# Kernel tuning notes

Hardware: AMD Instinct MI355X
Metric: run time of the kernel (lower is better)

The kernel has to match this reference:

```python
import jax, jax.numpy as jnp
import numpy as np
from math import log

MODEL_DIM = 512
NUM_HEADS = 8
DIM_HEAD = 64
INNER = NUM_HEADS * DIM_HEAD
B, L = 8, 1024
EPS = 1e-5


def setup_inputs() -> dict:
    key = jax.random.key(0)
    ks = jax.random.split(key, 9)
    x = jax.random.normal(ks[0], (B, L, MODEL_DIM), dtype=jnp.float32)
    gamma = jnp.ones((MODEL_DIM,), jnp.float32)
    beta = jnp.zeros((MODEL_DIM,), jnp.float32)
    w_qkv = jax.random.normal(ks[1], (3 * INNER, MODEL_DIM), jnp.float32) * (MODEL_DIM ** -0.5)
    b_qkv = jnp.zeros((3 * INNER,), jnp.float32)
    w_pos = jax.random.normal(ks[2], (INNER, MODEL_DIM), jnp.float32) * (MODEL_DIM ** -0.5)
    w_out = jax.random.normal(ks[3], (MODEL_DIM, INNER), jnp.float32) * (INNER ** -0.5)
    b_out = jnp.zeros((MODEL_DIM,), jnp.float32)
    # xavier_uniform for (num_heads, dim_head)
    bound = (6.0 / (NUM_HEADS + DIM_HEAD)) ** 0.5
    u_bias = jax.random.uniform(ks[4], (NUM_HEADS, DIM_HEAD), jnp.float32, -bound, bound)
    v_bias = jax.random.uniform(ks[5], (NUM_HEADS, DIM_HEAD), jnp.float32, -bound, bound)
    return {"x": x, "gamma": gamma, "beta": beta, "w_qkv": w_qkv, "b_qkv": b_qkv,
            "w_pos": w_pos, "w_out": w_out, "b_out": b_out, "u_bias": u_bias, "v_bias": v_bias}


def _rel_pos_emb(seq_len, d):
    # (L, D): (i - j) scaled by sinusoid frequencies, then cos on even cols, sin on odd cols
    rel = (jnp.arange(seq_len, dtype=jnp.float32)[:, None]
           - jnp.arange(d, dtype=jnp.float32)[None, :])
    freqs = jnp.exp(-jnp.arange(0, 2 * d, 2, dtype=jnp.float32) * (log(10000.0) / MODEL_DIM))
    angle = rel * freqs[None, :]
    even = (jnp.arange(d) % 2) == 0
    return jnp.where(even[None, :], jnp.cos(angle), jnp.sin(angle))  # (L, D)


def reference(x, gamma, beta, w_qkv, b_qkv, w_pos, w_out, b_out, u_bias, v_bias):
    b, l, d = x.shape
    h, dh = NUM_HEADS, DIM_HEAD
    # LayerNorm
    mu = jnp.mean(x, axis=-1, keepdims=True)
    var = jnp.mean(jnp.square(x - mu), axis=-1, keepdims=True)
    xn = (x - mu) * jax.lax.rsqrt(var + EPS) * gamma + beta
    # relative position embedding, identical per batch element
    pe = _rel_pos_emb(l, d)                      # (L, D)
    pos = (pe @ w_pos.T).reshape(l, h, dh)       # (L, H, Dh)
    pos = jnp.transpose(pos, (1, 0, 2))          # (H, L, Dh)
    # qkv
    qkv = xn @ w_qkv.T + b_qkv                   # (B, L, 3*inner)
    q, k, v = jnp.split(qkv, 3, axis=-1)
    def to_heads(t):
        return jnp.transpose(t.reshape(b, l, h, dh), (0, 2, 1, 3))  # (B,H,L,Dh)
    q, k, v = to_heads(q), to_heads(k), to_heads(v)
    scale = dh ** -0.5
    content = jnp.einsum('bhld,bhmd->bhlm', q + u_bias[None, :, None, :], k)
    pos_score = jnp.einsum('bhld,hmd->bhlm', q + v_bias[None, :, None, :], pos)
    attn = jax.nn.softmax((content + pos_score) * scale, axis=-1)
    out = jnp.einsum('bhlm,bhmd->bhld', attn, v)
    out = jnp.transpose(out, (0, 2, 1, 3)).reshape(b, l, h * dh)
    return out @ w_out.T + b_out  # dropout p=0.0 -> identity
```

## Files before the change

### kernel.cpp

```cpp
#include <hip/hip_runtime.h>
#include <math.h>

static constexpr int Bn = 8, Ln = 1024, Dm = 512, Hn = 8, DhN = 64;

typedef short bf16x8 __attribute__((ext_vector_type(8)));
typedef float f32x4 __attribute__((ext_vector_type(4)));
typedef _Float16 f16x4 __attribute__((ext_vector_type(4)));
typedef _Float16 f16x8 __attribute__((ext_vector_type(8)));
typedef unsigned int u32x4 __attribute__((ext_vector_type(4)));
typedef unsigned short u16x8 __attribute__((ext_vector_type(8)));

#define QSCALE 0.1803368801111137f

static __device__ __forceinline__ unsigned short f2b(float f) {
  union { float f; unsigned int u; } x;
  x.f = f;
  unsigned int u = x.u;
  unsigned int r = (u + 0x7FFFu + ((u >> 16) & 1u)) >> 16;
  return (unsigned short)r;
}
static __device__ __forceinline__ float b2f(unsigned short u) {
  union { unsigned int u; float f; } x;
  x.u = ((unsigned int)u) << 16;
  return x.f;
}

#define GLDS16(g, l)                                                        \
  __builtin_amdgcn_global_load_lds((const __attribute__((address_space(1))) void*)(g), \
                                   (__attribute__((address_space(3))) void*)(l), 16, 0, 0)

__global__ __launch_bounds__(256) void prep1(const float* __restrict__ x,
                                             const float* __restrict__ gamma,
                                             const float* __restrict__ beta,
                                             unsigned short* __restrict__ xn,
                                             unsigned short* __restrict__ pe,
                                             const float* __restrict__ wq, unsigned short* __restrict__ wqb,
                                             const float* __restrict__ wp, unsigned short* __restrict__ wpb,
                                             const float* __restrict__ wo, unsigned short* __restrict__ wob) {
  int b = blockIdx.x;
  int t = threadIdx.x;
  if (b < 4096) {
    int row = b * 2 + (t >> 7);
    int tl = t & 127;
    const float4 v = *(const float4*)(x + (size_t)row * Dm + tl * 4);
    float s = v.x + v.y + v.z + v.w;
    float sq = v.x * v.x + v.y * v.y + v.z * v.z + v.w * v.w;
#pragma unroll
    for (int off = 32; off > 0; off >>= 1) {
      s += __shfl_down(s, off);
      sq += __shfl_down(sq, off);
    }
    __shared__ float red[8];
    int wave = t >> 6, lane = t & 63;
    if (lane == 0) { red[wave * 2] = s; red[wave * 2 + 1] = sq; }
    __syncthreads();
    int half = t >> 7;
    float S = red[half * 4 + 0] + red[half * 4 + 2];
    float SQ = red[half * 4 + 1] + red[half * 4 + 3];
    float mu = S * (1.0f / Dm);
    float var = SQ * (1.0f / Dm) - mu * mu;
    float rstd = rsqrtf(var + 1e-5f);
    int c = tl * 4;
    const float4 g4 = *(const float4*)(gamma + c);
    const float4 b4 = *(const float4*)(beta + c);
    ushort4 o;
    o.x = f2b((v.x - mu) * rstd * g4.x + b4.x);
    o.y = f2b((v.y - mu) * rstd * g4.y + b4.y);
    o.z = f2b((v.z - mu) * rstd * g4.z + b4.z);
    o.w = f2b((v.w - mu) * rstd * g4.w + b4.w);
    *(ushort4*)(xn + (size_t)row * Dm + c) = o;
  } else if (b < 6144) {
    int idx = (b - 4096) * 256 + t;
    int l = idx >> 9, k = idx & 511;
    float freq = __expf(-0.0359778921f * (float)k);
    float angle = (float)(l - k) * freq;
    pe[idx] = f2b((k & 1) ? __sinf(angle) : __cosf(angle));
  } else {
    int cb = b - 6144;
    const float* src;
    unsigned short* dst;
    int off;
    if (cb < 768) { src = wq; dst = wqb; off = cb; }
    else if (cb < 1024) { src = wp; dst = wpb; off = cb - 768; }
    else { src = wo; dst = wob; off = cb - 1024; }
    int i = off * 256 + t;
    float4 v = *(const float4*)(src + (size_t)i * 4);
    ushort4 o;
    o.x = f2b(v.x); o.y = f2b(v.y); o.z = f2b(v.z); o.w = f2b(v.w);
    *(ushort4*)(dst + (size_t)i * 4) = o;
  }
}

__global__ __launch_bounds__(256, 5) void gemm2(const unsigned short* __restrict__ Ain,
                                                const unsigned short* __restrict__ Bwin,
                                                const float* __restrict__ biasin,
                                                unsigned short* __restrict__ oq,
                                                unsigned short* __restrict__ ok,
                                                unsigned short* __restrict__ ov,
                                                const unsigned short* __restrict__ A2,
                                                const unsigned short* __restrict__ B2,
                                                unsigned short* __restrict__ outp) {
  int by = blockIdx.y, bx = blockIdx.x;
  int mode = 0;
  const unsigned short* A = Ain;
  const unsigned short* Bw = Bwin;
  const float* bias = biasin;
  if (by < 128) {
    int lid = by * 24 + bx;
    int i = lid >> 3;
    by = (lid & 7) * 16 + i / 24;
    bx = i % 24;
  } else {
    if (bx >= 8) return;
    A = A2; Bw = B2; bias = nullptr; mode = 1; by -= 128;
  }
  const int K = 512;
  __shared__ alignas(16) unsigned short As[64 * 128];
  __shared__ alignas(16) unsigned short Bs[64 * 128];
  const int t = threadIdx.x;
  const int lane = t & 63, w = t >> 6;
  const int c = lane & 15, q8 = lane >> 4;
  const int wm = (w & 1) * 32, wn = (w >> 1) * 32;
  const int m0 = by * 64, n0 = bx * 64;

  f32x4 acc[2][2];
#pragma unroll
  for (int i = 0; i < 2; ++i)
#pragma unroll
    for (int j = 0; j < 2; ++j) acc[i][j] = (f32x4){0.f, 0.f, 0.f, 0.f};

  const int srow = t >> 4;
  const int sgr = (t & 15) ^ srow;

  for (int k0 = 0; k0 < K; k0 += 128) {
    __syncthreads();
#pragma unroll
    for (int p = 0; p < 4; ++p) {
      int r = p * 16 + srow;
      GLDS16(A + (size_t)(m0 + r) * K + k0 + sgr * 8, As + (p * 256 + t) * 8);
      GLDS16(Bw + (size_t)(n0 + r) * K + k0 + sgr * 8, Bs + (p * 256 + t) * 8);
    }
    __syncthreads();
#pragma unroll
    for (int kk = 0; kk < 4; ++kk) {
      bf16x8 a[2], b[2];
      const int q = kk * 4 + q8;
#pragma unroll
      for (int i = 0; i < 2; ++i) {
        int r = wm + i * 16 + c;
        a[i] = *(const bf16x8*)&As[(r * 16 + (q ^ (r & 15))) * 8];
      }
#pragma unroll
      for (int j = 0; j < 2; ++j) {
        int r = wn + j * 16 + c;
        b[j] = *(const bf16x8*)&Bs[(r * 16 + (q ^ (r & 15))) * 8];
      }
#pragma unroll
      for (int i = 0; i < 2; ++i)
#pragma unroll
        for (int j = 0; j < 2; ++j)
          acc[i][j] = __builtin_amdgcn_mfma_f32_16x16x32_bf16(a[i], b[j], acc[i][j], 0, 0, 0);
    }
  }
#pragma unroll
  for (int i = 0; i < 2; ++i) {
#pragma unroll
    for (int r = 0; r < 4; ++r) {
      int m = m0 + wm + i * 16 + q8 * 4 + r;
#pragma unroll
      for (int j = 0; j < 2; ++j) {
        int n = n0 + wn + j * 16 + c;
        float val = acc[i][j][r] + (bias ? bias[n] : 0.0f);
        if (mode == 0) {
          int part = n >> 9, h = (n >> 6) & 7, dh = n & 63;
          int bb = m >> 10, l = m & 1023;
          size_t idx = (size_t)((bb * 8 + h) * 1024 + l) * 64 + dh;
          if (part == 0) {
            oq[idx] = f2b(val * QSCALE);
          } else if (part == 1) {
            ok[idx] = f2b(val);
          } else {
            union { _Float16 h; unsigned short u; } cv;
            cv.h = (_Float16)val;
            ov[idx] = cv.u;
          }
        } else {
          int h = n >> 6, dh = n & 63;
          outp[(size_t)(h * 1024 + m) * 64 + dh] = f2b(val);
        }
      }
    }
  }
}

__global__ __launch_bounds__(256, 8) void gemm_mfma(const unsigned short* __restrict__ Ain,
                                                    const unsigned short* __restrict__ Bwin,
                                                    const float* __restrict__ biasin,
                                                    float* __restrict__ outfin,
                                                    int K) {
  int by = blockIdx.y, bx = blockIdx.x;
  {
    int NBX = gridDim.x;
    int lid = by * NBX + bx;
    int i = lid >> 3;
    by = (lid & 7) * 16 + i / NBX;
    bx = i % NBX;
  }
  const unsigned short* A = Ain;
  const unsigned short* Bw = Bwin;
  const float* bias = biasin;
  float* outf = outfin;
  __shared__ alignas(16) unsigned short As[64 * 64];
  __shared__ alignas(16) unsigned short Bs[64 * 64];
  const int t = threadIdx.x;
  const int lane = t & 63, w = t >> 6;
  const int c = lane & 15, q8 = lane >> 4;
  const int wm = (w & 1) * 32, wn = (w >> 1) * 32;
  const int m0 = by * 64, n0 = bx * 64;

  f32x4 acc[2][2];
#pragma unroll
  for (int i = 0; i < 2; ++i)
#pragma unroll
    for (int j = 0; j < 2; ++j) acc[i][j] = (f32x4){0.f, 0.f, 0.f, 0.f};

  const int srow = lane >> 3;
  const int sgr = (lane & 7) ^ srow;

  for (int k0 = 0; k0 < K; k0 += 64) {
    __syncthreads();
#pragma unroll
    for (int j = 0; j < 2; ++j) {
      int r = j * 32 + w * 8 + srow;
      GLDS16(A + (size_t)(m0 + r) * K + k0 + sgr * 8, As + (j * 256 + w * 64 + lane) * 8);
      GLDS16(Bw + (size_t)(n0 + r) * K + k0 + sgr * 8, Bs + (j * 256 + w * 64 + lane) * 8);
    }
    __syncthreads();
#pragma unroll
    for (int kk = 0; kk < 2; ++kk) {
      bf16x8 a[2], b[2];
      const int q = kk * 4 + q8;
#pragma unroll
      for (int i = 0; i < 2; ++i) {
        int r = wm + i * 16 + c;
        a[i] = *(const bf16x8*)&As[(r * 8 + (q ^ (r & 7))) * 8];
      }
#pragma unroll
      for (int j = 0; j < 2; ++j) {
        int r = wn + j * 16 + c;
        b[j] = *(const bf16x8*)&Bs[(r * 8 + (q ^ (r & 7))) * 8];
      }
#pragma unroll
      for (int i = 0; i < 2; ++i)
#pragma unroll
        for (int j = 0; j < 2; ++j)
          acc[i][j] = __builtin_amdgcn_mfma_f32_16x16x32_bf16(a[i], b[j], acc[i][j], 0, 0, 0);
    }
  }
#pragma unroll
  for (int i = 0; i < 2; ++i) {
#pragma unroll
    for (int r = 0; r < 4; ++r) {
      int m = m0 + wm + i * 16 + q8 * 4 + r;
#pragma unroll
      for (int j = 0; j < 2; ++j) {
        int n = n0 + wn + j * 16 + c;
        outf[(size_t)m * 512 + n] = acc[i][j][r] + bias[n];
      }
    }
  }
}

__global__ __launch_bounds__(256) void prep2(unsigned short* __restrict__ kbuf,
                                             const unsigned short* __restrict__ posbf,
                                             const float* __restrict__ ub,
                                             const float* __restrict__ vbb,
                                             float* __restrict__ biasout,
                                             const unsigned short* __restrict__ v,
                                             unsigned short* __restrict__ vt) {
  int b = blockIdx.x;
  int t = threadIdx.x;
  if (b < 2048) {
    int g = b * 32 + (t >> 3);
    int s = t & 7;
    int h = (g >> 10) & 7;
    int m = g & 1023;
    u16x8 kv8 = *(const u16x8*)(kbuf + (size_t)g * 64 + s * 8);
    u16x8 pv8 = *(const u16x8*)(posbf + (size_t)(h * 1024 + m) * 64 + s * 8);
    f32x4 u0 = *(const f32x4*)(ub + h * 64 + s * 8);
    f32x4 u1 = *(const f32x4*)(ub + h * 64 + s * 8 + 4);
    f32x4 v0 = *(const f32x4*)(vbb + h * 64 + s * 8);
    f32x4 v1 = *(const f32x4*)(vbb + h * 64 + s * 8 + 4);
    float part = 0.0f;
    u16x8 o8;
#pragma unroll
    for (int e = 0; e < 8; ++e) {
      float kf = b2f(kv8[e]);
      float pf = b2f(pv8[e]);
      float ue = (e < 4) ? u0[e] : u1[e - 4];
      float ve = (e < 4) ? v0[e] : v1[e - 4];
      part += ue * kf + ve * pf;
      o8[e] = f2b(kf + pf);
    }
    *(u16x8*)(kbuf + (size_t)g * 64 + s * 8) = o8;
    part += __shfl_xor(part, 1);
    part += __shfl_xor(part, 2);
    part += __shfl_xor(part, 4);
    if (s == 0) biasout[g] = part * QSCALE;
  } else {
    __shared__ unsigned short Ts[64 * 68];
    int bb = b - 2048;
    int bh = bb >> 4, lt = bb & 15;
    const unsigned short* vg = v + (size_t)bh * 65536 + lt * 4096;
#pragma unroll
    for (int s = 0; s < 4; ++s) {
      int idx = t + s * 256;
      int r = idx >> 4, c4 = (idx & 15) << 2;
      *(ushort4*)&Ts[r * 68 + c4] = *(const ushort4*)(vg + r * 64 + c4);
    }
    __syncthreads();
#pragma unroll
    for (int s = 0; s < 4; ++s) {
      int idx = t + s * 256;
      int d = idx >> 4, l4 = (idx & 15) << 2;
      ushort4 o;
      o.x = Ts[(l4 + 0) * 68 + d];
      o.y = Ts[(l4 + 1) * 68 + d];
      o.z = Ts[(l4 + 2) * 68 + d];
      o.w = Ts[(l4 + 3) * 68 + d];
      int pb = ((l4 >> 5) & 1) * 32 + ((l4 >> 2) & 3) * 8 + ((l4 >> 4) & 1) * 4;
      *(ushort4*)(vt + (size_t)bh * 65536 + d * 1024 + lt * 64 + pb) = o;
    }
  }
}

__global__ __launch_bounds__(256, 2) void flash_mfma(const unsigned short* __restrict__ qbf,
                                                     const unsigned short* __restrict__ kbf,
                                                     const unsigned short* __restrict__ vt,
                                                     const float* __restrict__ bias,
                                                     unsigned short* __restrict__ attn_out) {
  __shared__ alignas(16) unsigned short Ks[2][64 * 64];
  __shared__ alignas(16) unsigned short Vs[2][64 * 64];
  __shared__ alignas(16) float Bls[1024];
  const int t = threadIdx.x;
  const int lane = t & 63, w = t >> 6;
  const int c = lane & 15, q8 = lane >> 4;
  const int cc7 = c & 7;
  const int lid = blockIdx.x + (blockIdx.y << 3);
  const int bh = ((lid & 7) << 3) + ((lid >> 3) & 7);
  const int qt = lid >> 6;
  const unsigned short* qg = qbf + (size_t)bh * 65536;
  const unsigned short* kg = kbf + (size_t)bh * 65536;
  const unsigned short* vg = vt + (size_t)bh * 65536;
  const float* bg = bias + (size_t)bh * 1024;

  GLDS16(bg + t * 4, Bls + t * 4);

  bf16x8 bq[2][2];
#pragma unroll
  for (int g = 0; g < 2; ++g) {
    int qlg = qt * 128 + g * 64 + w * 16 + c;
    bq[g][0] = *(const bf16x8*)(qg + (size_t)qlg * 64 + q8 * 8);
    bq[g][1] = *(const bf16x8*)(qg + (size_t)qlg * 64 + 32 + q8 * 8);
  }

  float m_st[2] = {-INFINITY, -INFINITY};
  float l_st[2] = {0.0f, 0.0f};
  f32x4 o[2][4];
#pragma unroll
  for (int g = 0; g < 2; ++g)
#pragma unroll
    for (int i = 0; i < 4; ++i) o[g][i] = (f32x4){0.f, 0.f, 0.f, 0.f};

  const int srow = lane >> 3;
  const int sgr = (lane & 7) ^ srow;
  const int r0 = w * 16 + srow;

  u32x4 pk[2][2], pv[2][2];
#pragma unroll
  for (int h = 0; h < 2; ++h)
#pragma unroll
    for (int j = 0; j < 2; ++j) {
      int r = r0 + j * 8;
      pk[h][j] = *(const u32x4*)(kg + (size_t)(h * 64 + r) * 64 + sgr * 8);
      pv[h][j] = *(const u32x4*)(vg + (size_t)r * 1024 + h * 64 + sgr * 8);
    }

  for (int it = 0; it < 8; ++it) {
    __syncthreads();
#pragma unroll
    for (int h = 0; h < 2; ++h)
#pragma unroll
      for (int j = 0; j < 2; ++j) {
        int r = r0 + j * 8;
        *(u32x4*)&Ks[h][(r * 8 + (lane & 7)) * 8] = pk[h][j];
        *(u32x4*)&Vs[h][(r * 8 + (lane & 7)) * 8] = pv[h][j];
      }
    __syncthreads();
    if (it < 7) {
#pragma unroll
      for (int h = 0; h < 2; ++h)
#pragma unroll
        for (int j = 0; j < 2; ++j) {
          int r = r0 + j * 8;
          pk[h][j] = *(const u32x4*)(kg + (size_t)((it + 1) * 128 + h * 64 + r) * 64 + sgr * 8);
          pv[h][j] = *(const u32x4*)(vg + (size_t)r * 1024 + (it + 1) * 128 + h * 64 + sgr * 8);
        }
    }

    f32x4 sc[2][2][4];
#pragma unroll
    for (int h = 0; h < 2; ++h) {
#pragma unroll
      for (int nt = 0; nt < 4; ++nt) {
        f32x4 ci = *(const f32x4*)&Bls[it * 128 + h * 64 + nt * 16 + q8 * 4];
        const int row = nt * 16 + c;
        bf16x8 ak0 = *(const bf16x8*)&Ks[h][(row * 8 + (q8 ^ cc7)) * 8];
        bf16x8 ak1 = *(const bf16x8*)&Ks[h][(row * 8 + ((q8 + 4) ^ cc7)) * 8];
#pragma unroll
        for (int g = 0; g < 2; ++g) {
          f32x4 z = __builtin_amdgcn_mfma_f32_16x16x32_bf16(ak0, bq[g][0], ci, 0, 0, 0);
          sc[g][h][nt] = __builtin_amdgcn_mfma_f32_16x16x32_bf16(ak1, bq[g][1], z, 0, 0, 0);
        }
      }
    }
    float mx[2];
#pragma unroll
    for (int g = 0; g < 2; ++g) {
      float m = sc[g][0][0][0];
#pragma unroll
      for (int h = 0; h < 2; ++h)
#pragma unroll
        for (int nt = 0; nt < 4; ++nt)
#pragma unroll
          for (int r = 0; r < 4; ++r) m = fmaxf(m, sc[g][h][nt][r]);
      mx[g] = m;
    }
    {
      float s0 = __shfl_xor(mx[0], 16);
      float s1 = __shfl_xor(mx[1], 16);
      mx[0] = fmaxf(mx[0], s0);
      mx[1] = fmaxf(mx[1], s1);
      s0 = __shfl_xor(mx[0], 32);
      s1 = __shfl_xor(mx[1], 32);
      mx[0] = fmaxf(mx[0], s0);
      mx[1] = fmaxf(mx[1], s1);
    }
    f16x8 pf8[2][2][2];
#pragma unroll
    for (int g = 0; g < 2; ++g) {
      float mn = fmaxf(m_st[g], mx[g]);
      float al = __builtin_amdgcn_exp2f(m_st[g] - mn);
      float su = 0.0f;
#pragma unroll
      for (int h = 0; h < 2; ++h)
#pragma unroll
        for (int nt = 0; nt < 4; ++nt)
#pragma unroll
          for (int r = 0; r < 4; ++r) {
            float p = __builtin_amdgcn_exp2f(sc[g][h][nt][r] - mn);
            su += p;
            pf8[g][h][nt >> 1][((nt & 1) << 2) | r] = (_Float16)p;
          }
      l_st[g] = l_st[g] * al + su;
      m_st[g] = mn;
#pragma unroll
      for (int i = 0; i < 4; ++i) o[g][i] *= al;
    }
#pragma unroll
    for (int i = 0; i < 4; ++i) {
      const int row = i * 16 + c;
#pragma unroll
      for (int h = 0; h < 2; ++h) {
        f16x8 va = *(const f16x8*)&Vs[h][(row * 8 + (q8 ^ cc7)) * 8];
        f16x8 vb = *(const f16x8*)&Vs[h][(row * 8 + ((4 + q8) ^ cc7)) * 8];
#pragma unroll
        for (int g = 0; g < 2; ++g) {
          o[g][i] = __builtin_amdgcn_mfma_f32_16x16x32_f16(va, pf8[g][h][0], o[g][i], 0, 0, 0);
          o[g][i] = __builtin_amdgcn_mfma_f32_16x16x32_f16(vb, pf8[g][h][1], o[g][i], 0, 0, 0);
        }
      }
    }
  }
  float lt0 = l_st[0], lt1 = l_st[1];
  {
    float s0 = __shfl_xor(lt0, 16);
    float s1 = __shfl_xor(lt1, 16);
    lt0 += s0; lt1 += s1;
    s0 = __shfl_xor(lt0, 32);
    s1 = __shfl_xor(lt1, 32);
    lt0 += s0; lt1 += s1;
  }
  const int bidx = bh >> 3, h = bh & 7;
#pragma unroll
  for (int g = 0; g < 2; ++g) {
    int qlg = qt * 128 + g * 64 + w * 16 + c;
    float inv = 1.0f / (g == 0 ? lt0 : lt1);
    size_t base = (size_t)(bidx * 1024 + qlg) * 512 + h * 64;
#pragma unroll
    for (int i = 0; i < 4; ++i) {
      ushort4 ov4;
      ov4.x = f2b(o[g][i][0] * inv);
      ov4.y = f2b(o[g][i][1] * inv);
      ov4.z = f2b(o[g][i][2] * inv);
      ov4.w = f2b(o[g][i][3] * inv);
      *(ushort4*)(attn_out + base + i * 16 + q8 * 4) = ov4;
    }
  }
}

extern "C" void kernel_launch(void* const* d_in, const int* in_sizes, int n_in,
                              void* d_out, int out_size, void* d_ws, size_t ws_size,
                              hipStream_t stream) {
  const float* x      = (const float*)d_in[0];
  const float* gamma  = (const float*)d_in[1];
  const float* beta   = (const float*)d_in[2];
  const float* w_qkv  = (const float*)d_in[3];
  const float* b_qkv  = (const float*)d_in[4];
  const float* w_pos  = (const float*)d_in[5];
  const float* w_out  = (const float*)d_in[6];
  const float* b_out  = (const float*)d_in[7];
  const float* u_bias = (const float*)d_in[8];
  const float* v_bias = (const float*)d_in[9];
  float* out = (float*)d_out;

  unsigned short* wsu = (unsigned short*)d_ws;
  unsigned short* xnb   = wsu;
  unsigned short* peb   = wsu + 4194304;
  unsigned short* wqkvb = wsu + 4718592;
  unsigned short* wposb = wsu + 5505024;
  unsigned short* woutb = wsu + 5767168;
  unsigned short* qbf   = wsu + 6291456;
  unsigned short* kbf   = wsu + 10485760;
  unsigned short* vbf   = wsu + 14680064;
  unsigned short* vtb   = wsu + 18874368;
  unsigned short* attnb = wsu + 23068672;
  unsigned short* posbf = wsu + 27262976;
  float* biasb = (float*)(wsu + 28311552);

  prep1<<<7424, 256, 0, stream>>>(x, gamma, beta, xnb, peb,
                                  w_qkv, wqkvb, w_pos, wposb, w_out, woutb);
  gemm2<<<dim3(24, 144), 256, 0, stream>>>(xnb, wqkvb, b_qkv, qbf, kbf, vbf,
                                           peb, wposb, posbf);
  prep2<<<3072, 256, 0, stream>>>(kbf, posbf, u_bias, v_bias, biasb, vbf, vtb);
  flash_mfma<<<dim3(8, 64), 256, 0, stream>>>(qbf, kbf, vtb, biasb, attnb);
  gemm_mfma<<<dim3(8, 128), 256, 0, stream>>>(attnb, woutb, b_out, out, 512);
}
```

Baseline: 163.3 us.

## Fold positional projection into augmented K GEMM and fuse V transpose epilogue

```diff
diff --git a/kernel.cpp b/kernel.cpp
--- a/kernel.cpp
+++ b/kernel.cpp
@@ -32,11 +32,19 @@
 __global__ __launch_bounds__(256) void prep1(const float* __restrict__ x,
                                              const float* __restrict__ gamma,
                                              const float* __restrict__ beta,
+                                             const float* __restrict__ wq,
+                                             const float* __restrict__ wp,
+                                             const float* __restrict__ wo,
+                                             const float* __restrict__ bq,
+                                             const float* __restrict__ ub,
+                                             const float* __restrict__ vb,
                                              unsigned short* __restrict__ xn,
                                              unsigned short* __restrict__ pe,
-                                             const float* __restrict__ wq, unsigned short* __restrict__ wqb,
-                                             const float* __restrict__ wp, unsigned short* __restrict__ wpb,
-                                             const float* __restrict__ wo, unsigned short* __restrict__ wob) {
+                                             unsigned short* __restrict__ wqb,
+                                             unsigned short* __restrict__ wob,
+                                             unsigned short* __restrict__ wkaug,
+                                             unsigned short* __restrict__ wbias,
+                                             float* __restrict__ ubkb) {
   int b = blockIdx.x;
   int t = threadIdx.x;
   if (b < 4096) {
@@ -75,53 +83,93 @@
     float freq = __expf(-0.0359778921f * (float)k);
     float angle = (float)(l - k) * freq;
     pe[idx] = f2b((k & 1) ? __sinf(angle) : __cosf(angle));
-  } else {
+  } else if (b < 7168) {
     int cb = b - 6144;
     const float* src;
     unsigned short* dst;
     int off;
     if (cb < 768) { src = wq; dst = wqb; off = cb; }
-    else if (cb < 1024) { src = wp; dst = wpb; off = cb - 768; }
-    else { src = wo; dst = wob; off = cb - 1024; }
+    else { src = wo; dst = wob; off = cb - 768; }
     int i = off * 256 + t;
     float4 v = *(const float4*)(src + (size_t)i * 4);
     ushort4 o;
     o.x = f2b(v.x); o.y = f2b(v.y); o.z = f2b(v.z); o.w = f2b(v.w);
     *(ushort4*)(dst + (size_t)i * 4) = o;
-  }
-}
-
-__global__ __launch_bounds__(256, 5) void gemm2(const unsigned short* __restrict__ Ain,
-                                                const unsigned short* __restrict__ Bwin,
-                                                const float* __restrict__ biasin,
+  } else if (b < 7424) {
+    int i = (b - 7168) * 256 + t;
+    int e = i * 4, r = e >> 9, c = e & 511;
+    float4 v = *(const float4*)(wq + (size_t)(512 + r) * 512 + c);
+    ushort4 o;
+    o.x = f2b(v.x); o.y = f2b(v.y); o.z = f2b(v.z); o.w = f2b(v.w);
+    *(ushort4*)(wkaug + (size_t)r * 1024 + c) = o;
+  } else if (b < 7680) {
+    int i = (b - 7424) * 256 + t;
+    int e = i * 4, r = e >> 9, c = e & 511;
+    float4 v = *(const float4*)(wp + (size_t)r * 512 + c);
+    ushort4 o;
+    o.x = f2b(v.x); o.y = f2b(v.y); o.z = f2b(v.z); o.w = f2b(v.w);
+    *(ushort4*)(wkaug + (size_t)r * 1024 + 512 + c) = o;
+  } else if (b < 7688) {
+    int h = b - 7680;
+    int k4 = t * 4;
+    float a0 = 0.f, a1 = 0.f, a2 = 0.f, a3 = 0.f;
+    for (int dh = 0; dh < 64; ++dh) {
+      float s;
+      const float* wr;
+      if (k4 < 512) { s = ub[h * 64 + dh]; wr = wq + (size_t)(512 + h * 64 + dh) * 512 + k4; }
+      else { s = vb[h * 64 + dh]; wr = wp + (size_t)(h * 64 + dh) * 512 + (k4 - 512); }
+      float4 w4 = *(const float4*)wr;
+      a0 += s * w4.x; a1 += s * w4.y; a2 += s * w4.z; a3 += s * w4.w;
+    }
+    ushort4 o;
+    o.x = f2b(a0); o.y = f2b(a1); o.z = f2b(a2); o.w = f2b(a3);
+    *(ushort4*)(wbias + h * 1024 + k4) = o;
+    if (t < 64) {
+      float pu = ub[h * 64 + t] * bq[512 + h * 64 + t];
+#pragma unroll
+      for (int off = 32; off > 0; off >>= 1) pu += __shfl_down(pu, off);
+      if (t == 0) ubkb[h] = pu;
+    }
+  } else {
+    int row = 8 + (b - 7688);
+    ushort4 z = {0, 0, 0, 0};
+    *(ushort4*)(wbias + row * 1024 + t * 4) = z;
+  }
+}
+
+__global__ __launch_bounds__(256, 5) void gemm3(const unsigned short* __restrict__ xn,
+                                                const unsigned short* __restrict__ pe,
+                                                const unsigned short* __restrict__ wqb,
+                                                const unsigned short* __restrict__ wkaug,
+                                                const unsigned short* __restrict__ wbias,
+                                                const float* __restrict__ bq,
+                                                const float* __restrict__ ubkb,
                                                 unsigned short* __restrict__ oq,
                                                 unsigned short* __restrict__ ok,
-                                                unsigned short* __restrict__ ov,
-                                                const unsigned short* __restrict__ A2,
-                                                const unsigned short* __restrict__ B2,
-                                                unsigned short* __restrict__ outp) {
+                                                unsigned short* __restrict__ vtb,
+                                                float* __restrict__ biasb) {
   int by = blockIdx.y, bx = blockIdx.x;
-  int mode = 0;
-  const unsigned short* A = Ain;
-  const unsigned short* Bw = Bwin;
-  const float* bias = biasin;
-  if (by < 128) {
-    int lid = by * 24 + bx;
+  {
+    int lid = by * 25 + bx;
     int i = lid >> 3;
-    by = (lid & 7) * 16 + i / 24;
-    bx = i % 24;
-  } else {
-    if (bx >= 8) return;
-    A = A2; Bw = B2; bias = nullptr; mode = 1; by -= 128;
-  }
-  const int K = 512;
+    by = (lid & 7) * 16 + i / 25;
+    bx = i % 25;
+  }
+  int part, brow, KK, bstride;
+  const unsigned short* Bw;
+  if (bx < 8) { part = 0; Bw = wqb; brow = bx * 64; KK = 512; bstride = 512; }
+  else if (bx < 16) { part = 1; Bw = wkaug; brow = (bx - 8) * 64; KK = 1024; bstride = 1024; }
+  else if (bx < 24) { part = 2; Bw = wqb + (size_t)1024 * 512; brow = (bx - 16) * 64; KK = 512; bstride = 512; }
+  else { part = 3; Bw = wbias; brow = 0; KK = 1024; bstride = 1024; }
+
   __shared__ alignas(16) unsigned short As[64 * 128];
   __shared__ alignas(16) unsigned short Bs[64 * 128];
   const int t = threadIdx.x;
   const int lane = t & 63, w = t >> 6;
   const int c = lane & 15, q8 = lane >> 4;
   const int wm = (w & 1) * 32, wn = (w >> 1) * 32;
-  const int m0 = by * 64, n0 = bx * 64;
+  const int m0 = by * 64;
+  const int b_ = m0 >> 10, l0 = m0 & 1023;
 
   f32x4 acc[2][2];
 #pragma unroll
@@ -132,13 +180,16 @@
   const int srow = t >> 4;
   const int sgr = (t & 15) ^ srow;
 
-  for (int k0 = 0; k0 < K; k0 += 128) {
+  for (int k0 = 0; k0 < KK; k0 += 128) {
     __syncthreads();
 #pragma unroll
     for (int p = 0; p < 4; ++p) {
       int r = p * 16 + srow;
-      GLDS16(A + (size_t)(m0 + r) * K + k0 + sgr * 8, As + (p * 256 + t) * 8);
-      GLDS16(Bw + (size_t)(n0 + r) * K + k0 + sgr * 8, Bs + (p * 256 + t) * 8);
+      const unsigned short* asrc =
+          (k0 < 512) ? xn + (size_t)(m0 + r) * 512 + k0 + sgr * 8
+                     : pe + (size_t)(l0 + r) * 512 + (k0 - 512) + sgr * 8;
+      GLDS16(asrc, As + (p * 256 + t) * 8);
+      GLDS16(Bw + (size_t)(brow + r) * bstride + k0 + sgr * 8, Bs + (p * 256 + t) * 8);
     }
     __syncthreads();
 #pragma unroll
@@ -162,34 +213,74 @@
           acc[i][j] = __builtin_amdgcn_mfma_f32_16x16x32_bf16(a[i], b[j], acc[i][j], 0, 0, 0);
     }
   }
-#pragma unroll
-  for (int i = 0; i < 2; ++i) {
-#pragma unroll
-    for (int r = 0; r < 4; ++r) {
-      int m = m0 + wm + i * 16 + q8 * 4 + r;
-#pragma unroll
-      for (int j = 0; j < 2; ++j) {
-        int n = n0 + wn + j * 16 + c;
-        float val = acc[i][j][r] + (bias ? bias[n] : 0.0f);
-        if (mode == 0) {
-          int part = n >> 9, h = (n >> 6) & 7, dh = n & 63;
-          int bb = m >> 10, l = m & 1023;
-          size_t idx = (size_t)((bb * 8 + h) * 1024 + l) * 64 + dh;
+
+  if (part == 2) {
+    unsigned short* Ts = As;
+    __syncthreads();
+#pragma unroll
+    for (int i = 0; i < 2; ++i)
+#pragma unroll
+      for (int r = 0; r < 4; ++r) {
+        int ar = wm + i * 16 + q8 * 4 + r;
+#pragma unroll
+        for (int j = 0; j < 2; ++j) {
+          int ac = wn + j * 16 + c;
+          float val = acc[i][j][r] + bq[1024 + brow + ac];
+          union { _Float16 hv; unsigned short u; } cv;
+          cv.hv = (_Float16)val;
+          Ts[ar * 68 + ac] = cv.u;
+        }
+      }
+    __syncthreads();
+    int bh_ = b_ * 8 + (brow >> 6);
+    int lt = l0 >> 6;
+#pragma unroll
+    for (int s = 0; s < 4; ++s) {
+      int idx = t + s * 256;
+      int d = idx >> 4, l4 = (idx & 15) << 2;
+      ushort4 o4;
+      o4.x = Ts[(l4 + 0) * 68 + d];
+      o4.y = Ts[(l4 + 1) * 68 + d];
+      o4.z = Ts[(l4 + 2) * 68 + d];
+      o4.w = Ts[(l4 + 3) * 68 + d];
+      int pb = ((l4 >> 5) & 1) * 32 + ((l4 >> 2) & 3) * 8 + ((l4 >> 4) & 1) * 4;
+      *(ushort4*)(vtb + (size_t)bh_ * 65536 + d * 1024 + lt * 64 + pb) = o4;
+    }
+  } else if (part == 3) {
+#pragma unroll
+    for (int i = 0; i < 2; ++i)
+#pragma unroll
+      for (int r = 0; r < 4; ++r) {
+        int m = m0 + wm + i * 16 + q8 * 4 + r;
+#pragma unroll
+        for (int j = 0; j < 2; ++j) {
+          int col = wn + j * 16 + c;
+          if (col < 8) {
+            float val = acc[i][j][r] + ubkb[col];
+            biasb[(size_t)(b_ * 8 + col) * 1024 + (m & 1023)] = val * QSCALE;
+          }
+        }
+      }
+  } else {
+#pragma unroll
+    for (int i = 0; i < 2; ++i)
+#pragma unroll
+      for (int r = 0; r < 4; ++r) {
+        int m = m0 + wm + i * 16 + q8 * 4 + r;
+        int l = m & 1023;
+#pragma unroll
+        for (int j = 0; j < 2; ++j) {
+          int ln = brow + wn + j * 16 + c;
+          int h = ln >> 6, dh = ln & 63;
+          float val = acc[i][j][r];
+          size_t idx = ((size_t)(b_ * 8 + h) * 1024 + l) * 64 + dh;
           if (part == 0) {
-            oq[idx] = f2b(val * QSCALE);
-          } else if (part == 1) {
-            ok[idx] = f2b(val);
+            oq[idx] = f2b((val + bq[ln]) * QSCALE);
           } else {
-            union { _Float16 h; unsigned short u; } cv;
-            cv.h = (_Float16)val;
-            ov[idx] = cv.u;
+            ok[idx] = f2b(val + bq[512 + ln]);
           }
-        } else {
-          int h = n >> 6, dh = n & 63;
-          outp[(size_t)(h * 1024 + m) * 64 + dh] = f2b(val);
         }
       }
-    }
   }
 }
 
@@ -267,69 +358,6 @@
         int n = n0 + wn + j * 16 + c;
         outf[(size_t)m * 512 + n] = acc[i][j][r] + bias[n];
       }
-    }
-  }
-}
-
-__global__ __launch_bounds__(256) void prep2(unsigned short* __restrict__ kbuf,
-                                             const unsigned short* __restrict__ posbf,
-                                             const float* __restrict__ ub,
-                                             const float* __restrict__ vbb,
-                                             float* __restrict__ biasout,
-                                             const unsigned short* __restrict__ v,
-                                             unsigned short* __restrict__ vt) {
-  int b = blockIdx.x;
-  int t = threadIdx.x;
-  if (b < 2048) {
-    int g = b * 32 + (t >> 3);
-    int s = t & 7;
-    int h = (g >> 10) & 7;
-    int m = g & 1023;
-    u16x8 kv8 = *(const u16x8*)(kbuf + (size_t)g * 64 + s * 8);
-    u16x8 pv8 = *(const u16x8*)(posbf + (size_t)(h * 1024 + m) * 64 + s * 8);
-    f32x4 u0 = *(const f32x4*)(ub + h * 64 + s * 8);
-    f32x4 u1 = *(const f32x4*)(ub + h * 64 + s * 8 + 4);
-    f32x4 v0 = *(const f32x4*)(vbb + h * 64 + s * 8);
-    f32x4 v1 = *(const f32x4*)(vbb + h * 64 + s * 8 + 4);
-    float part = 0.0f;
-    u16x8 o8;
-#pragma unroll
-    for (int e = 0; e < 8; ++e) {
-      float kf = b2f(kv8[e]);
-      float pf = b2f(pv8[e]);
-      float ue = (e < 4) ? u0[e] : u1[e - 4];
-      float ve = (e < 4) ? v0[e] : v1[e - 4];
-      part += ue * kf + ve * pf;
-      o8[e] = f2b(kf + pf);
-    }
-    *(u16x8*)(kbuf + (size_t)g * 64 + s * 8) = o8;
-    part += __shfl_xor(part, 1);
-    part += __shfl_xor(part, 2);
-    part += __shfl_xor(part, 4);
-    if (s == 0) biasout[g] = part * QSCALE;
-  } else {
-    __shared__ unsigned short Ts[64 * 68];
-    int bb = b - 2048;
-    int bh = bb >> 4, lt = bb & 15;
-    const unsigned short* vg = v + (size_t)bh * 65536 + lt * 4096;
-#pragma unroll
-    for (int s = 0; s < 4; ++s) {
-      int idx = t + s * 256;
-      int r = idx >> 4, c4 = (idx & 15) << 2;
-      *(ushort4*)&Ts[r * 68 + c4] = *(const ushort4*)(vg + r * 64 + c4);
-    }
-    __syncthreads();
-#pragma unroll
-    for (int s = 0; s < 4; ++s) {
-      int idx = t + s * 256;
-      int d = idx >> 4, l4 = (idx & 15) << 2;
-      ushort4 o;
-      o.x = Ts[(l4 + 0) * 68 + d];
-      o.y = Ts[(l4 + 1) * 68 + d];
-      o.z = Ts[(l4 + 2) * 68 + d];
-      o.w = Ts[(l4 + 3) * 68 + d];
-      int pb = ((l4 >> 5) & 1) * 32 + ((l4 >> 2) & 3) * 8 + ((l4 >> 4) & 1) * 4;
-      *(ushort4*)(vt + (size_t)bh * 65536 + d * 1024 + lt * 64 + pb) = o;
     }
   }
 }
@@ -528,21 +556,20 @@
   unsigned short* xnb   = wsu;
   unsigned short* peb   = wsu + 4194304;
   unsigned short* wqkvb = wsu + 4718592;
-  unsigned short* wposb = wsu + 5505024;
-  unsigned short* woutb = wsu + 5767168;
-  unsigned short* qbf   = wsu + 6291456;
-  unsigned short* kbf   = wsu + 10485760;
-  unsigned short* vbf   = wsu + 14680064;
-  unsigned short* vtb   = wsu + 18874368;
-  unsigned short* attnb = wsu + 23068672;
-  unsigned short* posbf = wsu + 27262976;
-  float* biasb = (float*)(wsu + 28311552);
-
-  prep1<<<7424, 256, 0, stream>>>(x, gamma, beta, xnb, peb,
-                                  w_qkv, wqkvb, w_pos, wposb, w_out, woutb);
-  gemm2<<<dim3(24, 144), 256, 0, stream>>>(xnb, wqkvb, b_qkv, qbf, kbf, vbf,
-                                           peb, wposb, posbf);
-  prep2<<<3072, 256, 0, stream>>>(kbf, posbf, u_bias, v_bias, biasb, vbf, vtb);
+  unsigned short* woutb = wsu + 5505024;
+  unsigned short* wkaug = wsu + 5767168;
+  unsigned short* wbias = wsu + 6291456;
+  unsigned short* qbf   = wsu + 6356992;
+  unsigned short* kbf   = wsu + 10551296;
+  unsigned short* vtb   = wsu + 14745600;
+  unsigned short* attnb = wsu + 18939904;
+  float* biasb = (float*)(wsu + 23134208);
+  float* ubkb  = (float*)(wsu + 23265280);
+
+  prep1<<<7744, 256, 0, stream>>>(x, gamma, beta, w_qkv, w_pos, w_out, b_qkv, u_bias, v_bias,
+                                  xnb, peb, wqkvb, woutb, wkaug, wbias, ubkb);
+  gemm3<<<dim3(25, 128), 256, 0, stream>>>(xnb, peb, wqkvb, wkaug, wbias, b_qkv, ubkb,
+                                           qbf, kbf, vtb, biasb);
   flash_mfma<<<dim3(8, 64), 256, 0, stream>>>(qbf, kbf, vtb, biasb, attnb);
   gemm_mfma<<<dim3(8, 128), 256, 0, stream>>>(attnb, woutb, b_out, out, 512);
 }
```

Measured after the change: 169.1 us. +3.5%, slower.
